# Performance work log

Measured on AMD Instinct MI355X. Metric: run time of the kernel, lower is better.

## Reference

```python
import jax, jax.numpy as jnp
import numpy as np

VOCAB = 21128
D_WENLAN = 2048
SENT_LEN = 44  # hard-coded in original forward


def setup_inputs() -> dict:
    key = jax.random.key(0)
    ks = jax.random.split(key, 8)
    B, S, P = 32, 8, 32
    L = S * SENT_LEN  # 352
    concat_output = jax.random.normal(ks[0], (B, S, D_WENLAN), jnp.float32)
    input_ids = jax.random.randint(ks[1], (B, L), 0, VOCAB, jnp.int32)
    topic_ids = jax.random.randint(ks[2], (B, P), 0, VOCAB, jnp.int32)
    tpw_att_mask = jnp.ones((B, P), jnp.int32)
    tpw_type_ids = jnp.zeros((B, P), jnp.int32)
    attention_mask = jnp.ones((B, L), jnp.int32)
    type_ids = jax.random.randint(ks[3], (B, L), 0, 8, jnp.int32)
    token_table = jax.random.normal(ks[4], (VOCAB, D_WENLAN), jnp.float32) * 0.02
    W1 = jax.random.normal(ks[5], (D_WENLAN, 512), jnp.float32) * 0.02
    b1 = jnp.zeros((512,), jnp.float32)
    W2 = jax.random.normal(ks[6], (512, 768), jnp.float32) * 0.02
    b2 = jnp.zeros((768,), jnp.float32)
    return dict(concat_output=concat_output, input_ids=input_ids, topic_ids=topic_ids,
                tpw_att_mask=tpw_att_mask, tpw_type_ids=tpw_type_ids,
                attention_mask=attention_mask, type_ids=type_ids,
                token_table=token_table, W1=W1, b1=b1, W2=W2, b2=b2)


def reference(concat_output, input_ids, topic_ids, tpw_att_mask, tpw_type_ids,
              attention_mask, type_ids, token_table, W1, b1, W2, b2):
    B, S, D = concat_output.shape
    # vectorized replacement of the python double-loop dict lookups:
    topic_emb = token_table[topic_ids]                      # [B,P,2048]
    inp_emb = token_table[input_ids]                        # [B,L,2048]
    # scatter-add: each sentence block of 44 tokens gets its concat_output row added
    inp_emb = inp_emb.reshape(B, S, SENT_LEN, D) + concat_output[:, :, None, :]
    input_embs = jnp.concatenate([topic_emb, inp_emb.reshape(B, S * SENT_LEN, D)], axis=1)
    # projector MLP (Linear -> tanh -> Linear)
    h = jnp.tanh(jnp.einsum('btd,dk->btk', input_embs, W1) + b1)
    gpt_input_embs = jnp.einsum('btk,ke->bte', h, W2) + b2   # [B,P+L,768]
    # auxiliary concatenated tensors fed to gpt2 (is_train=True path)
    labels = jnp.concatenate([topic_ids, input_ids], axis=1)
    full_type_ids = jnp.concatenate([tpw_type_ids, type_ids], axis=1)
    full_att_mask = jnp.concatenate([tpw_att_mask, attention_mask], axis=1)
    return gpt_input_embs, labels, full_type_ids, full_att_mask
```

## Files before the change

### kernel.cpp

```cpp
#include <hip/hip_runtime.h>
#include <math.h>

typedef _Float16 half8 __attribute__((ext_vector_type(8)));
typedef float f32x4 __attribute__((ext_vector_type(4)));

#define BB 32
#define SS 8
#define PP 32
#define SENT 44
#define LL 352
#define TT 384
#define DD 2048
#define H1 512
#define H2 768
#define MM (BB*TT)
#define OUT0 (MM*H2)

#define GLL16(g, l) __builtin_amdgcn_global_load_lds( \
    (const __attribute__((address_space(1))) void*)(g), \
    (__attribute__((address_space(3))) void*)(l), 16, 0, 0)

__global__ __launch_bounds__(256) void gather_kernel(
    const float* __restrict__ token_table,
    const int*   __restrict__ topic_ids,
    const int*   __restrict__ input_ids,
    const float* __restrict__ concat_output,
    _Float16*    __restrict__ A16)
{
    const int m = blockIdx.x;
    const int b = m / TT;
    const int t = m % TT;
    const float* src;
    const float* addp = nullptr;
    if (t < PP) {
        src = token_table + (size_t)topic_ids[b * PP + t] * DD;
    } else {
        int u = t - PP;
        src = token_table + (size_t)input_ids[b * LL + u] * DD;
        addp = concat_output + ((size_t)b * SS + (u / SENT)) * DD;
    }
    _Float16* dst = A16 + (size_t)m * DD;
    const int base = threadIdx.x * 8;
    float4 v0 = *(const float4*)(src + base);
    float4 v1 = *(const float4*)(src + base + 4);
    if (addp) {
        float4 c0 = *(const float4*)(addp + base);
        float4 c1 = *(const float4*)(addp + base + 4);
        v0.x += c0.x; v0.y += c0.y; v0.z += c0.z; v0.w += c0.w;
        v1.x += c1.x; v1.y += c1.y; v1.z += c1.z; v1.w += c1.w;
    }
    half8 h;
    h[0] = (_Float16)v0.x; h[1] = (_Float16)v0.y; h[2] = (_Float16)v0.z; h[3] = (_Float16)v0.w;
    h[4] = (_Float16)v1.x; h[5] = (_Float16)v1.y; h[6] = (_Float16)v1.z; h[7] = (_Float16)v1.w;
    *(half8*)(dst + base) = h;
}

__global__ __launch_bounds__(256) void transpose_f16_kernel(
    const float* __restrict__ src, _Float16* __restrict__ dst, int R, int C)
{
    __shared__ float tile[32][33];
    int c0 = blockIdx.x * 32;
    int r0 = blockIdx.y * 32;
    int tx = threadIdx.x & 31;
    int ty = threadIdx.x >> 5;
    #pragma unroll
    for (int i = 0; i < 4; ++i)
        tile[ty + i*8][tx] = src[(size_t)(r0 + ty + i*8) * C + c0 + tx];
    __syncthreads();
    #pragma unroll
    for (int i = 0; i < 4; ++i)
        dst[(size_t)(c0 + ty + i*8) * R + r0 + tx] = (_Float16)tile[tx][ty + i*8];
}

__global__ __launch_bounds__(256) void gemm1_kernel(
    const _Float16* __restrict__ A16,
    const _Float16* __restrict__ W1T,
    const float*    __restrict__ b1,
    _Float16*       __restrict__ Hout)
{
    const int tid  = threadIdx.x;
    const int wid  = tid >> 6;
    const int lane = tid & 63;

    const int logical = ((blockIdx.x & 7) * 96) + (blockIdx.x >> 3);
    const int bm = logical >> 2;
    const int bn = logical & 3;

    __shared__ _Float16 As[2][64 * 64];
    __shared__ _Float16 Bs[2][128 * 64];

    const int lrow = lane >> 3;
    const int lcol = (lane & 7) * 8;
    const _Float16* ag0 = A16 + (size_t)(bm * 64 + wid * 8       + lrow) * DD + lcol;
    const _Float16* ag1 = A16 + (size_t)(bm * 64 + (wid + 4) * 8 + lrow) * DD + lcol;
    const _Float16* bg0 = W1T + (size_t)(bn * 128 +  wid       * 8 + lrow) * DD + lcol;
    const _Float16* bg1 = W1T + (size_t)(bn * 128 + (wid +  4) * 8 + lrow) * DD + lcol;
    const _Float16* bg2 = W1T + (size_t)(bn * 128 + (wid +  8) * 8 + lrow) * DD + lcol;
    const _Float16* bg3 = W1T + (size_t)(bn * 128 + (wid + 12) * 8 + lrow) * DD + lcol;

    #define G1_ISSUE(buf, k0) {                                        \
        GLL16(ag0 + (k0), &As[buf][ wid      * 512]);                  \
        GLL16(ag1 + (k0), &As[buf][(wid + 4) * 512]);                  \
        GLL16(bg0 + (k0), &Bs[buf][ wid       * 512]);                 \
        GLL16(bg1 + (k0), &Bs[buf][(wid +  4) * 512]);                 \
        GLL16(bg2 + (k0), &Bs[buf][(wid +  8) * 512]);                 \
        GLL16(bg3 + (k0), &Bs[buf][(wid + 12) * 512]);                 \
    }

    const int wrow = (wid >> 1) * 32;
    const int wcol = (wid & 1) * 64;
    const int fr   = lane & 15;
    const int fg   = lane >> 4;

    f32x4 acc[2][4] = {};

    G1_ISSUE(0, 0);

    const int NT = DD / 64;
    for (int t = 0; t < NT; ++t) {
        __syncthreads();
        if (t + 1 < NT) G1_ISSUE((t + 1) & 1, (t + 1) * 64);
        const int cb = t & 1;
        #pragma unroll
        for (int kk = 0; kk < 2; ++kk) {
            half8 af[2], bf[4];
            #pragma unroll
            for (int i = 0; i < 2; ++i)
                af[i] = *(const half8*)&As[cb][(wrow + i*16 + fr) * 64 + kk*32 + fg*8];
            #pragma unroll
            for (int j = 0; j < 4; ++j)
                bf[j] = *(const half8*)&Bs[cb][(wcol + j*16 + fr) * 64 + kk*32 + fg*8];
            #pragma unroll
            for (int i = 0; i < 2; ++i)
                #pragma unroll
                for (int j = 0; j < 4; ++j)
                    acc[i][j] = __builtin_amdgcn_mfma_f32_16x16x32_f16(af[i], bf[j], acc[i][j], 0, 0, 0);
        }
    }

    #pragma unroll
    for (int i = 0; i < 2; ++i) {
        #pragma unroll
        for (int j = 0; j < 4; ++j) {
            int col = bn * 128 + wcol + j * 16 + fr;
            float bias = b1[col];
            #pragma unroll
            for (int r = 0; r < 4; ++r) {
                int row = bm * 64 + wrow + i * 16 + fg * 4 + r;
                Hout[(size_t)row * H1 + col] = (_Float16)tanhf(acc[i][j][r] + bias);
            }
        }
    }
    #undef G1_ISSUE
}

__global__ __launch_bounds__(256) void gemm2_kernel(
    const _Float16* __restrict__ Hin,
    const _Float16* __restrict__ W2T,
    const float*    __restrict__ b2,
    float*          __restrict__ out)
{
    const int tid  = threadIdx.x;
    const int wid  = tid >> 6;
    const int lane = tid & 63;

    const int logical = ((blockIdx.x & 7) * 72) + (blockIdx.x >> 3);
    const int bm = logical / 6;
    const int bn = logical % 6;

    __shared__ _Float16 As[2][128 * 64];
    __shared__ _Float16 Bs[2][128 * 64];

    const int lrow = lane >> 3;
    const int lcol = (lane & 7) * 8;
    const _Float16* ag[4];
    const _Float16* bg[4];
    #pragma unroll
    for (int q = 0; q < 4; ++q) {
        ag[q] = Hin + (size_t)(bm * 128 + (wid + q * 4) * 8 + lrow) * H1 + lcol;
        bg[q] = W2T + (size_t)(bn * 128 + (wid + q * 4) * 8 + lrow) * H1 + lcol;
    }

    #define G2_ISSUE(buf, k0) {                                        \
        _Pragma("unroll")                                              \
        for (int q = 0; q < 4; ++q) {                                  \
            GLL16(ag[q] + (k0), &As[buf][(wid + q * 4) * 512]);        \
            GLL16(bg[q] + (k0), &Bs[buf][(wid + q * 4) * 512]);        \
        }                                                              \
    }

    const int wrow = (wid >> 1) * 64;
    const int wcol = (wid & 1) * 64;
    const int fr   = lane & 15;
    const int fg   = lane >> 4;

    f32x4 acc[4][4] = {};

    G2_ISSUE(0, 0);

    const int NT = H1 / 64;
    for (int t = 0; t < NT; ++t) {
        __syncthreads();
        if (t + 1 < NT) G2_ISSUE((t + 1) & 1, (t + 1) * 64);
        const int cb = t & 1;
        #pragma unroll
        for (int kk = 0; kk < 2; ++kk) {
            half8 af[4], bf[4];
            #pragma unroll
            for (int i = 0; i < 4; ++i)
                af[i] = *(const half8*)&As[cb][(wrow + i*16 + fr) * 64 + kk*32 + fg*8];
            #pragma unroll
            for (int j = 0; j < 4; ++j)
                bf[j] = *(const half8*)&Bs[cb][(wcol + j*16 + fr) * 64 + kk*32 + fg*8];
            #pragma unroll
            for (int i = 0; i < 4; ++i)
                #pragma unroll
                for (int j = 0; j < 4; ++j)
                    acc[i][j] = __builtin_amdgcn_mfma_f32_16x16x32_f16(af[i], bf[j], acc[i][j], 0, 0, 0);
        }
    }

    #pragma unroll
    for (int i = 0; i < 4; ++i) {
        #pragma unroll
        for (int j = 0; j < 4; ++j) {
            int col = bn * 128 + wcol + j * 16 + fr;
            float bias = b2[col];
            #pragma unroll
            for (int r = 0; r < 4; ++r) {
                int row = bm * 128 + wrow + i * 16 + fg * 4 + r;
                out[(size_t)row * H2 + col] = acc[i][j][r] + bias;
            }
        }
    }
    #undef G2_ISSUE
}

__global__ __launch_bounds__(256) void aux_kernel(
    const int* __restrict__ topic_ids,
    const int* __restrict__ input_ids,
    const int* __restrict__ tpw_type_ids,
    const int* __restrict__ type_ids,
    const int* __restrict__ tpw_att_mask,
    const int* __restrict__ attention_mask,
    float* __restrict__ out)
{
    int idx = blockIdx.x * 256 + threadIdx.x;
    if (idx >= MM) return;
    int b = idx / TT, t = idx % TT;
    int lab, ty, mk;
    if (t < PP) {
        lab = topic_ids[b * PP + t];
        ty  = tpw_type_ids[b * PP + t];
        mk  = tpw_att_mask[b * PP + t];
    } else {
        int u = t - PP;
        lab = input_ids[b * LL + u];
        ty  = type_ids[b * LL + u];
        mk  = attention_mask[b * LL + u];
    }
    out[OUT0 + idx]          = (float)lab;
    out[OUT0 + MM + idx]     = (float)ty;
    out[OUT0 + 2 * MM + idx] = (float)mk;
}

extern "C" void kernel_launch(void* const* d_in, const int* in_sizes, int n_in,
                              void* d_out, int out_size, void* d_ws, size_t ws_size,
                              hipStream_t stream) {
    const float* concat_output  = (const float*)d_in[0];
    const int*   input_ids      = (const int*)d_in[1];
    const int*   topic_ids      = (const int*)d_in[2];
    const int*   tpw_att_mask   = (const int*)d_in[3];
    const int*   tpw_type_ids   = (const int*)d_in[4];
    const int*   attention_mask = (const int*)d_in[5];
    const int*   type_ids       = (const int*)d_in[6];
    const float* token_table    = (const float*)d_in[7];
    const float* W1             = (const float*)d_in[8];
    const float* b1             = (const float*)d_in[9];
    const float* W2             = (const float*)d_in[10];
    const float* b2             = (const float*)d_in[11];
    float* out = (float*)d_out;

    _Float16* w1t = (_Float16*)d_ws;
    _Float16* w2t = w1t + (size_t)H1 * DD;
    _Float16* Hws = w2t + (size_t)H2 * H1;
    _Float16* A16 = Hws + (size_t)MM * H1;

    transpose_f16_kernel<<<dim3(H1 / 32, DD / 32), 256, 0, stream>>>(W1, w1t, DD, H1);
    transpose_f16_kernel<<<dim3(H2 / 32, H1 / 32), 256, 0, stream>>>(W2, w2t, H1, H2);
    aux_kernel<<<(MM + 255) / 256, 256, 0, stream>>>(
        topic_ids, input_ids, tpw_type_ids, type_ids, tpw_att_mask, attention_mask, out);
    gather_kernel<<<MM, 256, 0, stream>>>(
        token_table, topic_ids, input_ids, concat_output, A16);

    gemm1_kernel<<<(MM / 64) * (H1 / 128), 256, 0, stream>>>(A16, w1t, b1, Hws);
    gemm2_kernel<<<(MM / 128) * (H2 / 128), 256, 0, stream>>>(Hws, w2t, b2, out);
}
```

Baseline: 114.8 us.

## Fuse embedding gather into GEMM1 with register-staged A and swizzled LDS

Drops the separate gather kernel and the fp16 A16 intermediate. GEMM1 now reads token-table rows (plus concat_output) directly in fp32, converts them to fp16 in registers and writes them to an XOR-swizzled LDS tile, pipelined across two buffers. The GEMM1 N-tile grows from 128 to 256, and both GEMMs use XOR swizzling to avoid LDS bank conflicts. This removes one full write and read of the large A matrix. In exchange GEMM1 reads fp32 table rows, which doubles the bytes per element, redoes the gather for each N tile, and uses more registers.

```diff
diff --git a/kernel.cpp b/kernel.cpp
--- a/kernel.cpp
+++ b/kernel.cpp
@@ -19,41 +19,6 @@
 #define GLL16(g, l) __builtin_amdgcn_global_load_lds( \
     (const __attribute__((address_space(1))) void*)(g), \
     (__attribute__((address_space(3))) void*)(l), 16, 0, 0)
-
-__global__ __launch_bounds__(256) void gather_kernel(
-    const float* __restrict__ token_table,
-    const int*   __restrict__ topic_ids,
-    const int*   __restrict__ input_ids,
-    const float* __restrict__ concat_output,
-    _Float16*    __restrict__ A16)
-{
-    const int m = blockIdx.x;
-    const int b = m / TT;
-    const int t = m % TT;
-    const float* src;
-    const float* addp = nullptr;
-    if (t < PP) {
-        src = token_table + (size_t)topic_ids[b * PP + t] * DD;
-    } else {
-        int u = t - PP;
-        src = token_table + (size_t)input_ids[b * LL + u] * DD;
-        addp = concat_output + ((size_t)b * SS + (u / SENT)) * DD;
-    }
-    _Float16* dst = A16 + (size_t)m * DD;
-    const int base = threadIdx.x * 8;
-    float4 v0 = *(const float4*)(src + base);
-    float4 v1 = *(const float4*)(src + base + 4);
-    if (addp) {
-        float4 c0 = *(const float4*)(addp + base);
-        float4 c1 = *(const float4*)(addp + base + 4);
-        v0.x += c0.x; v0.y += c0.y; v0.z += c0.z; v0.w += c0.w;
-        v1.x += c1.x; v1.y += c1.y; v1.z += c1.z; v1.w += c1.w;
-    }
-    half8 h;
-    h[0] = (_Float16)v0.x; h[1] = (_Float16)v0.y; h[2] = (_Float16)v0.z; h[3] = (_Float16)v0.w;
-    h[4] = (_Float16)v1.x; h[5] = (_Float16)v1.y; h[6] = (_Float16)v1.z; h[7] = (_Float16)v1.w;
-    *(half8*)(dst + base) = h;
-}
 
 __global__ __launch_bounds__(256) void transpose_f16_kernel(
     const float* __restrict__ src, _Float16* __restrict__ dst, int R, int C)
@@ -73,7 +38,10 @@
 }
 
 __global__ __launch_bounds__(256) void gemm1_kernel(
-    const _Float16* __restrict__ A16,
+    const float*    __restrict__ token_table,
+    const int*      __restrict__ topic_ids,
+    const int*      __restrict__ input_ids,
+    const float*    __restrict__ concat_output,
     const _Float16* __restrict__ W1T,
     const float*    __restrict__ b1,
     _Float16*       __restrict__ Hout)
@@ -82,67 +50,135 @@
     const int wid  = tid >> 6;
     const int lane = tid & 63;
 
-    const int logical = ((blockIdx.x & 7) * 96) + (blockIdx.x >> 3);
-    const int bm = logical >> 2;
-    const int bn = logical & 3;
+    const int logical = ((blockIdx.x & 7) * 48) + (blockIdx.x >> 3);
+    const int bm = logical >> 1;
+    const int bn = logical & 1;
 
     __shared__ _Float16 As[2][64 * 64];
-    __shared__ _Float16 Bs[2][128 * 64];
-
-    const int lrow = lane >> 3;
-    const int lcol = (lane & 7) * 8;
-    const _Float16* ag0 = A16 + (size_t)(bm * 64 + wid * 8       + lrow) * DD + lcol;
-    const _Float16* ag1 = A16 + (size_t)(bm * 64 + (wid + 4) * 8 + lrow) * DD + lcol;
-    const _Float16* bg0 = W1T + (size_t)(bn * 128 +  wid       * 8 + lrow) * DD + lcol;
-    const _Float16* bg1 = W1T + (size_t)(bn * 128 + (wid +  4) * 8 + lrow) * DD + lcol;
-    const _Float16* bg2 = W1T + (size_t)(bn * 128 + (wid +  8) * 8 + lrow) * DD + lcol;
-    const _Float16* bg3 = W1T + (size_t)(bn * 128 + (wid + 12) * 8 + lrow) * DD + lcol;
-
-    #define G1_ISSUE(buf, k0) {                                        \
-        GLL16(ag0 + (k0), &As[buf][ wid      * 512]);                  \
-        GLL16(ag1 + (k0), &As[buf][(wid + 4) * 512]);                  \
-        GLL16(bg0 + (k0), &Bs[buf][ wid       * 512]);                 \
-        GLL16(bg1 + (k0), &Bs[buf][(wid +  4) * 512]);                 \
-        GLL16(bg2 + (k0), &Bs[buf][(wid +  8) * 512]);                 \
-        GLL16(bg3 + (k0), &Bs[buf][(wid + 12) * 512]);                 \
+    __shared__ _Float16 Bs[2][256 * 64];
+
+    const int arow = tid >> 2;
+    const int akq  = (tid & 3) * 16;
+    const int aswz = (arow & 7) << 3;
+
+    {
+    }
+    const int m = bm * 64 + arow;
+    const int b = m / TT;
+    const int t = m % TT;
+    const float* aptr;
+    const float* addp = nullptr;
+    if (t < PP) {
+        aptr = token_table + (size_t)topic_ids[b * PP + t] * DD;
+    } else {
+        int u = t - PP;
+        aptr = token_table + (size_t)input_ids[b * LL + u] * DD;
+        addp = concat_output + ((size_t)b * SS + (u / SENT)) * DD;
+    }
+
+    const int rl = lane >> 3;
+    const int cg = lane & 7;
+    const _Float16* bsrc = W1T + (size_t)(bn * 256 + wid * 64 + rl) * DD
+                               + ((cg ^ rl) << 3);
+
+    #define G1B(buf, k0) {                                                 \
+        _Pragma("unroll")                                                  \
+        for (int q = 0; q < 8; ++q)                                        \
+            GLL16(bsrc + (size_t)q * 8 * DD + (k0),                        \
+                  &Bs[buf][(wid * 8 + q) * 512]);                          \
+    }
+
+    #define LOADA(S, k0) {                                                 \
+        const float* ap = aptr + (k0) + akq;                               \
+        float4 v0 = *(const float4*)(ap);                                  \
+        float4 v1 = *(const float4*)(ap + 4);                              \
+        float4 v2 = *(const float4*)(ap + 8);                              \
+        float4 v3 = *(const float4*)(ap + 12);                             \
+        if (addp) {                                                        \
+            const float* cp = addp + (k0) + akq;                           \
+            float4 c0 = *(const float4*)(cp);                              \
+            float4 c1 = *(const float4*)(cp + 4);                          \
+            float4 c2 = *(const float4*)(cp + 8);                          \
+            float4 c3 = *(const float4*)(cp + 12);                         \
+            v0.x += c0.x; v0.y += c0.y; v0.z += c0.z; v0.w += c0.w;        \
+            v1.x += c1.x; v1.y += c1.y; v1.z += c1.z; v1.w += c1.w;        \
+            v2.x += c2.x; v2.y += c2.y; v2.z += c2.z; v2.w += c2.w;        \
+            v3.x += c3.x; v3.y += c3.y; v3.z += c3.z; v3.w += c3.w;        \
+        }                                                                  \
+        S[0]=v0.x; S[1]=v0.y; S[2]=v0.z; S[3]=v0.w;                        \
+        S[4]=v1.x; S[5]=v1.y; S[6]=v1.z; S[7]=v1.w;                        \
+        S[8]=v2.x; S[9]=v2.y; S[10]=v2.z; S[11]=v2.w;                      \
+        S[12]=v3.x; S[13]=v3.y; S[14]=v3.z; S[15]=v3.w;                    \
+    }
+
+    #define WRITEA(S, buf) {                                               \
+        half8 h0, h1;                                                      \
+        _Pragma("unroll")                                                  \
+        for (int j = 0; j < 8; ++j) { h0[j] = (_Float16)S[j];              \
+                                      h1[j] = (_Float16)S[8 + j]; }        \
+        *(half8*)&As[buf][(arow * 64 + akq) ^ aswz]     = h0;              \
+        *(half8*)&As[buf][(arow * 64 + akq + 8) ^ aswz] = h1;              \
     }
 
     const int wrow = (wid >> 1) * 32;
-    const int wcol = (wid & 1) * 64;
+    const int wcol = (wid & 1) * 128;
     const int fr   = lane & 15;
     const int fg   = lane >> 4;
 
-    f32x4 acc[2][4] = {};
-
-    G1_ISSUE(0, 0);
-
-    const int NT = DD / 64;
-    for (int t = 0; t < NT; ++t) {
+    f32x4 acc[2][8] = {};
+
+    #define MFMAP(buf) {                                                   \
+        _Pragma("unroll")                                                  \
+        for (int kk = 0; kk < 2; ++kk) {                                   \
+            half8 af[2], bf[8];                                            \
+            _Pragma("unroll")                                              \
+            for (int i = 0; i < 2; ++i) {                                  \
+                int row = wrow + i * 16 + fr;                              \
+                af[i] = *(const half8*)&As[buf][                           \
+                    (row * 64 + kk * 32 + fg * 8) ^ ((row & 7) << 3)];     \
+            }                                                              \
+            _Pragma("unroll")                                              \
+            for (int j = 0; j < 8; ++j) {                                  \
+                int row = wcol + j * 16 + fr;                              \
+                bf[j] = *(const half8*)&Bs[buf][                           \
+                    (row * 64 + kk * 32 + fg * 8) ^ ((row & 7) << 3)];     \
+            }                                                              \
+            _Pragma("unroll")                                              \
+            for (int i = 0; i < 2; ++i)                                    \
+                _Pragma("unroll")                                          \
+                for (int j = 0; j < 8; ++j)                                \
+                    acc[i][j] = __builtin_amdgcn_mfma_f32_16x16x32_f16(    \
+                        af[i], bf[j], acc[i][j], 0, 0, 0);                 \
+        }                                                                  \
+    }
+
+    float a0[16], a1[16];
+
+    G1B(0, 0);
+    LOADA(a0, 0);
+    LOADA(a1, 64);
+    WRITEA(a0, 0);
+    __syncthreads();
+
+    for (int tt = 0; tt < 16; ++tt) {
+        const int t2 = tt * 2;
+        G1B(1, (t2 + 1) * 64);
+        if (t2 + 2 < 32) LOADA(a0, (t2 + 2) * 64);
+        MFMAP(0);
+        WRITEA(a1, 1);
         __syncthreads();
-        if (t + 1 < NT) G1_ISSUE((t + 1) & 1, (t + 1) * 64);
-        const int cb = t & 1;
-        #pragma unroll
-        for (int kk = 0; kk < 2; ++kk) {
-            half8 af[2], bf[4];
-            #pragma unroll
-            for (int i = 0; i < 2; ++i)
-                af[i] = *(const half8*)&As[cb][(wrow + i*16 + fr) * 64 + kk*32 + fg*8];
-            #pragma unroll
-            for (int j = 0; j < 4; ++j)
-                bf[j] = *(const half8*)&Bs[cb][(wcol + j*16 + fr) * 64 + kk*32 + fg*8];
-            #pragma unroll
-            for (int i = 0; i < 2; ++i)
-                #pragma unroll
-                for (int j = 0; j < 4; ++j)
-                    acc[i][j] = __builtin_amdgcn_mfma_f32_16x16x32_f16(af[i], bf[j], acc[i][j], 0, 0, 0);
-        }
+        if (t2 + 2 < 32) G1B(0, (t2 + 2) * 64);
+        if (t2 + 3 < 32) LOADA(a1, (t2 + 3) * 64);
+        MFMAP(1);
+        if (t2 + 2 < 32) WRITEA(a0, 0);
+        __syncthreads();
     }
 
     #pragma unroll
     for (int i = 0; i < 2; ++i) {
         #pragma unroll
-        for (int j = 0; j < 4; ++j) {
-            int col = bn * 128 + wcol + j * 16 + fr;
+        for (int j = 0; j < 8; ++j) {
+            int col = bn * 256 + wcol + j * 16 + fr;
             float bias = b1[col];
             #pragma unroll
             for (int r = 0; r < 4; ++r) {
@@ -151,7 +187,10 @@
             }
         }
     }
-    #undef G1_ISSUE
+    #undef G1B
+    #undef LOADA
+    #undef WRITEA
+    #undef MFMAP
 }
 
 __global__ __launch_bounds__(256) void gemm2_kernel(
@@ -171,22 +210,21 @@
     __shared__ _Float16 As[2][128 * 64];
     __shared__ _Float16 Bs[2][128 * 64];
 
-    const int lrow = lane >> 3;
-    const int lcol = (lane & 7) * 8;
-    const _Float16* ag[4];
-    const _Float16* bg[4];
-    #pragma unroll
-    for (int q = 0; q < 4; ++q) {
-        ag[q] = Hin + (size_t)(bm * 128 + (wid + q * 4) * 8 + lrow) * H1 + lcol;
-        bg[q] = W2T + (size_t)(bn * 128 + (wid + q * 4) * 8 + lrow) * H1 + lcol;
-    }
-
-    #define G2_ISSUE(buf, k0) {                                        \
-        _Pragma("unroll")                                              \
-        for (int q = 0; q < 4; ++q) {                                  \
-            GLL16(ag[q] + (k0), &As[buf][(wid + q * 4) * 512]);        \
-            GLL16(bg[q] + (k0), &Bs[buf][(wid + q * 4) * 512]);        \
-        }                                                              \
+    const int rl = lane >> 3;
+    const int cg = lane & 7;
+    const _Float16* asrc = Hin + (size_t)(bm * 128 + wid * 32 + rl) * H1
+                               + ((cg ^ rl) << 3);
+    const _Float16* bsrc = W2T + (size_t)(bn * 128 + wid * 32 + rl) * H1
+                               + ((cg ^ rl) << 3);
+
+    #define G2_ISSUE(buf, k0) {                                            \
+        _Pragma("unroll")                                                  \
+        for (int q = 0; q < 4; ++q) {                                      \
+            GLL16(asrc + (size_t)q * 8 * H1 + (k0),                        \
+                  &As[buf][(wid * 4 + q) * 512]);                          \
+            GLL16(bsrc + (size_t)q * 8 * H1 + (k0),                        \
+                  &Bs[buf][(wid * 4 + q) * 512]);                          \
+        }                                                                  \
     }
 
     const int wrow = (wid >> 1) * 64;
@@ -207,11 +245,17 @@
         for (int kk = 0; kk < 2; ++kk) {
             half8 af[4], bf[4];
             #pragma unroll
-            for (int i = 0; i < 4; ++i)
-                af[i] = *(const half8*)&As[cb][(wrow + i*16 + fr) * 64 + kk*32 + fg*8];
-            #pragma unroll
-            for (int j = 0; j < 4; ++j)
-                bf[j] = *(const half8*)&Bs[cb][(wcol + j*16 + fr) * 64 + kk*32 + fg*8];
+            for (int i = 0; i < 4; ++i) {
+                int row = wrow + i * 16 + fr;
+                af[i] = *(const half8*)&As[cb][
+                    (row * 64 + kk * 32 + fg * 8) ^ ((row & 7) << 3)];
+            }
+            #pragma unroll
+            for (int j = 0; j < 4; ++j) {
+                int row = wcol + j * 16 + fr;
+                bf[j] = *(const half8*)&Bs[cb][
+                    (row * 64 + kk * 32 + fg * 8) ^ ((row & 7) << 3)];
+            }
             #pragma unroll
             for (int i = 0; i < 4; ++i)
                 #pragma unroll
@@ -284,15 +328,13 @@
     _Float16* w1t = (_Float16*)d_ws;
     _Float16* w2t = w1t + (size_t)H1 * DD;
     _Float16* Hws = w2t + (size_t)H2 * H1;
-    _Float16* A16 = Hws + (size_t)MM * H1;
 
     transpose_f16_kernel<<<dim3(H1 / 32, DD / 32), 256, 0, stream>>>(W1, w1t, DD, H1);
     transpose_f16_kernel<<<dim3(H2 / 32, H1 / 32), 256, 0, stream>>>(W2, w2t, H1, H2);
     aux_kernel<<<(MM + 255) / 256, 256, 0, stream>>>(
         topic_ids, input_ids, tpw_type_ids, type_ids, tpw_att_mask, attention_mask, out);
-    gather_kernel<<<MM, 256, 0, stream>>>(
-        token_table, topic_ids, input_ids, concat_output, A16);
-
-    gemm1_kernel<<<(MM / 64) * (H1 / 128), 256, 0, stream>>>(A16, w1t, b1, Hws);
+
+    gemm1_kernel<<<(MM / 64) * (H1 / 256), 256, 0, stream>>>(
+        token_table, topic_ids, input_ids, concat_output, w1t, b1, Hws);
     gemm2_kernel<<<(MM / 128) * (H2 / 128), 256, 0, stream>>>(Hws, w2t, b2, out);
 }
```

Measured after the change: 104.3 us. -9.2%, faster.

## Widen gemm1 tile to 64x256 and XOR-swizzle LDS layout

Applied to the files above, without the earlier changes.

Gemm1 now computes a 64x256 output tile per block instead of 64x128, so each wave holds 2x8 MFMA accumulators and the A tile is reused across twice as many columns. The block count halves to 384, which lowers redundant A loads from global memory. Global-to-LDS loads and fragment reads now use an XOR swizzle on the column group to avoid LDS bank conflicts. The cost is double the B shared memory (about 80KB total with double buffering) and more accumulator registers, which may reduce occupancy.

```diff
diff --git a/kernel.cpp b/kernel.cpp
--- a/kernel.cpp
+++ b/kernel.cpp
@@ -82,37 +82,37 @@
     const int wid  = tid >> 6;
     const int lane = tid & 63;
 
-    const int logical = ((blockIdx.x & 7) * 96) + (blockIdx.x >> 3);
-    const int bm = logical >> 2;
-    const int bn = logical & 3;
+    const int logical = ((blockIdx.x & 7) * 48) + (blockIdx.x >> 3);
+    const int bm = logical >> 1;
+    const int bn = logical & 1;
 
     __shared__ _Float16 As[2][64 * 64];
-    __shared__ _Float16 Bs[2][128 * 64];
-
-    const int lrow = lane >> 3;
-    const int lcol = (lane & 7) * 8;
-    const _Float16* ag0 = A16 + (size_t)(bm * 64 + wid * 8       + lrow) * DD + lcol;
-    const _Float16* ag1 = A16 + (size_t)(bm * 64 + (wid + 4) * 8 + lrow) * DD + lcol;
-    const _Float16* bg0 = W1T + (size_t)(bn * 128 +  wid       * 8 + lrow) * DD + lcol;
-    const _Float16* bg1 = W1T + (size_t)(bn * 128 + (wid +  4) * 8 + lrow) * DD + lcol;
-    const _Float16* bg2 = W1T + (size_t)(bn * 128 + (wid +  8) * 8 + lrow) * DD + lcol;
-    const _Float16* bg3 = W1T + (size_t)(bn * 128 + (wid + 12) * 8 + lrow) * DD + lcol;
-
-    #define G1_ISSUE(buf, k0) {                                        \
-        GLL16(ag0 + (k0), &As[buf][ wid      * 512]);                  \
-        GLL16(ag1 + (k0), &As[buf][(wid + 4) * 512]);                  \
-        GLL16(bg0 + (k0), &Bs[buf][ wid       * 512]);                 \
-        GLL16(bg1 + (k0), &Bs[buf][(wid +  4) * 512]);                 \
-        GLL16(bg2 + (k0), &Bs[buf][(wid +  8) * 512]);                 \
-        GLL16(bg3 + (k0), &Bs[buf][(wid + 12) * 512]);                 \
+    __shared__ _Float16 Bs[2][256 * 64];
+
+    const int rl = lane >> 3;
+    const int cg = lane & 7;
+    const _Float16* asrc = A16 + (size_t)(bm * 64 + wid * 16 + rl) * DD
+                               + ((cg ^ rl) << 3);
+    const _Float16* bsrc = W1T + (size_t)(bn * 256 + wid * 64 + rl) * DD
+                               + ((cg ^ rl) << 3);
+
+    #define G1_ISSUE(buf, k0) {                                            \
+        _Pragma("unroll")                                                  \
+        for (int q = 0; q < 2; ++q)                                        \
+            GLL16(asrc + (size_t)q * 8 * DD + (k0),                        \
+                  &As[buf][(wid * 16 + q * 8) * 64]);                      \
+        _Pragma("unroll")                                                  \
+        for (int q = 0; q < 8; ++q)                                        \
+            GLL16(bsrc + (size_t)q * 8 * DD + (k0),                        \
+                  &Bs[buf][(wid * 64 + q * 8) * 64]);                      \
     }
 
     const int wrow = (wid >> 1) * 32;
-    const int wcol = (wid & 1) * 64;
+    const int wcol = (wid & 1) * 128;
     const int fr   = lane & 15;
     const int fg   = lane >> 4;
 
-    f32x4 acc[2][4] = {};
+    f32x4 acc[2][8] = {};
 
     G1_ISSUE(0, 0);
 
@@ -123,26 +123,33 @@
         const int cb = t & 1;
         #pragma unroll
         for (int kk = 0; kk < 2; ++kk) {
-            half8 af[2], bf[4];
-            #pragma unroll
-            for (int i = 0; i < 2; ++i)
-                af[i] = *(const half8*)&As[cb][(wrow + i*16 + fr) * 64 + kk*32 + fg*8];
-            #pragma unroll
-            for (int j = 0; j < 4; ++j)
-                bf[j] = *(const half8*)&Bs[cb][(wcol + j*16 + fr) * 64 + kk*32 + fg*8];
+            half8 af[2], bf[8];
+            #pragma unroll
+            for (int i = 0; i < 2; ++i) {
+                int row = wrow + i * 16 + fr;
+                af[i] = *(const half8*)&As[cb][
+                    (row * 64 + kk * 32 + fg * 8) ^ ((row & 7) << 3)];
+            }
+            #pragma unroll
+            for (int j = 0; j < 8; ++j) {
+                int row = wcol + j * 16 + fr;
+                bf[j] = *(const half8*)&Bs[cb][
+                    (row * 64 + kk * 32 + fg * 8) ^ ((row & 7) << 3)];
+            }
             #pragma unroll
             for (int i = 0; i < 2; ++i)
                 #pragma unroll
-                for (int j = 0; j < 4; ++j)
-                    acc[i][j] = __builtin_amdgcn_mfma_f32_16x16x32_f16(af[i], bf[j], acc[i][j], 0, 0, 0);
+                for (int j = 0; j < 8; ++j)
+                    acc[i][j] = __builtin_amdgcn_mfma_f32_16x16x32_f16(
+                        af[i], bf[j], acc[i][j], 0, 0, 0);
         }
     }
 
     #pragma unroll
     for (int i = 0; i < 2; ++i) {
         #pragma unroll
-        for (int j = 0; j < 4; ++j) {
-            int col = bn * 128 + wcol + j * 16 + fr;
+        for (int j = 0; j < 8; ++j) {
+            int col = bn * 256 + wcol + j * 16 + fr;
             float bias = b1[col];
             #pragma unroll
             for (int r = 0; r < 4; ++r) {
@@ -293,6 +300,6 @@
     gather_kernel<<<MM, 256, 0, stream>>>(
         token_table, topic_ids, input_ids, concat_output, A16);
 
-    gemm1_kernel<<<(MM / 64) * (H1 / 128), 256, 0, stream>>>(A16, w1t, b1, Hws);
+    gemm1_kernel<<<(MM / 64) * (H1 / 256), 256, 0, stream>>>(A16, w1t, b1, Hws);
     gemm2_kernel<<<(MM / 128) * (H2 / 128), 256, 0, stream>>>(Hws, w2t, b2, out);
 }
```

After: 121.4 us. +5.7%, slower.
